# Kernel tuning notes

Hardware: AMD Instinct MI355X
Metric: run time of the kernel (lower is better)

Reference implementation:

```python
import jax, jax.numpy as jnp
import numpy as np

B, T, D, H, N, S, FF = 8, 1024, 512, 8, 256, 256, 2048
AUD, TXT = 768, 256  # audio_input_dim, text_feature_dim (hardcoded in module)
EPS = 1e-5


def _ln(x, g, b):
    m = x.mean(-1, keepdims=True)
    v = ((x - m) ** 2).mean(-1, keepdims=True)
    return (x - m) / jnp.sqrt(v + EPS) * g + b


def _lin(x, w, b):
    return x @ w + b


def setup_inputs() -> dict:
    keys = iter(jax.random.split(jax.random.key(0), 64))
    def rn(shape, s=0.02):
        return jax.random.normal(next(keys), shape, jnp.float32) * s
    inp = {
        'x': jax.random.normal(next(keys), (B, T, D), jnp.float32),
        'xf': jax.random.normal(next(keys), (B, AUD), jnp.float32),
        'xw': jax.random.normal(next(keys), (B, N, TXT), jnp.float32),
        'xs': jax.random.normal(next(keys), (B, S, D), jnp.float32),
        # feat_proj (linear variant)
        'fp_w': rn((D, D)), 'fp_b': rn((D,)),
        # self-attention
        'sa_ng': 1.0 + rn((D,)), 'sa_nb': rn((D,)),
        'sa_qw': rn((D, D)), 'sa_qb': rn((D,)),
        'sa_kw': rn((D, D)), 'sa_kb': rn((D,)),
        'sa_vw': rn((D, D)), 'sa_vb': rn((D,)),
        'sa_ow': rn((D, D)), 'sa_ob': rn((D,)),
        # cross-attention
        'ca_ng': 1.0 + rn((D,)), 'ca_nb': rn((D,)),
        'ca_tng': 1.0 + rn((D,)), 'ca_tnb': rn((D,)),
        'ca_sng': 1.0 + rn((D,)), 'ca_snb': rn((D,)),
        'ca_qw': rn((D, D)), 'ca_qb': rn((D,)),
        'ca_kw': rn((D, D)), 'ca_kb': rn((D,)),
        'ca_vw': rn((D, D)), 'ca_vb': rn((D,)),
        'ca_apw': rn((AUD, TXT)), 'ca_apb': rn((TXT,)),
        'ca_atw': rn((TXT, D)), 'ca_atb': rn((D,)),
        'ca_ow': rn((D, D)), 'ca_ob': rn((D,)),
        'an_g': 1.0 + rn((D,)), 'an_b': rn((D,)),
        # FFN
        'ffn_w1': rn((D, FF)), 'ffn_b1': rn((FF,)),
        'ffn_w2': rn((FF, D)), 'ffn_b2': rn((D,)),
        'ffn_ng': 1.0 + rn((D,)), 'ffn_nb': rn((D,)),
        'ffn_ow': rn((D, D)), 'ffn_ob': rn((D,)),
    }
    return inp


def reference(x, xf, xw, xs, fp_w, fp_b, sa_ng, sa_nb, sa_qw, sa_qb, sa_kw, sa_kb,
              sa_vw, sa_vb, sa_ow, sa_ob, ca_ng, ca_nb, ca_tng, ca_tnb, ca_sng, ca_snb,
              ca_qw, ca_qb, ca_kw, ca_kb, ca_vw, ca_vb, ca_apw, ca_apb, ca_atw, ca_atb,
              ca_ow, ca_ob, an_g, an_b, ffn_w1, ffn_b1, ffn_w2, ffn_b2, ffn_ng, ffn_nb,
              ffn_ow, ffn_ob):
    Bx, Tx, Dx = x.shape
    dh = Dx // H
    # feat_proj + detached residual (x_ori = x.detach().clone())
    xp = _lin(x, fp_w, fp_b) + jax.lax.stop_gradient(x)

    # ---- self-attention block ----
    xn = _ln(xp, sa_ng, sa_nb)
    q = _lin(xn, sa_qw, sa_qb).reshape(Bx, Tx, H, dh)
    k = _lin(xn, sa_kw, sa_kb).reshape(Bx, Tx, H, dh)
    v = _lin(xn, sa_vw, sa_vb).reshape(Bx, Tx, H, dh)
    scores = jnp.einsum('bthd,bshd->bths', q, k) / jnp.sqrt(jnp.float32(dh))
    ao = jnp.einsum('bths,bshd->bthd', jax.nn.softmax(scores, -1), v).reshape(Bx, Tx, Dx)
    sa_out = xp + _lin(jax.nn.silu(ao), sa_ow, sa_ob)
    y1 = _ln(sa_out + xp, an_g, an_b)

    # ---- cross-attention block (linear attention over text/audio + semantic) ----
    Nw = xw.shape[1]
    xf_p = _lin(xf, ca_apw, ca_apb)                              # [B, 256]
    xf_e = jnp.broadcast_to(xf_p[:, None, :], (Bx, Nw, TXT))
    xw_xf = _lin(jnp.concatenate([xw, xf_e], axis=1), ca_atw, ca_atb)  # [B, 2N, D]
    tn = _ln(xw_xf, ca_tng, ca_tnb)
    sn = _ln(xs, ca_sng, ca_snb)
    cq = jax.nn.softmax(_lin(_ln(y1, ca_ng, ca_nb), ca_qw, ca_qb).reshape(Bx, Tx, H, dh), -1)
    ck = jax.nn.softmax(_lin(tn, ca_kw, ca_kb).reshape(Bx, 2 * Nw, H, dh), 1)
    sk = jax.nn.softmax(_lin(sn, ca_kw, ca_kb).reshape(Bx, -1, H, dh), 1)
    cv = _lin(tn, ca_vw, ca_vb).reshape(Bx, 2 * Nw, H, dh)
    sv = _lin(sn, ca_vw, ca_vb).reshape(Bx, -1, H, dh)
    att = jnp.einsum('bnhd,bnhl->bhdl', ck, cv)                  # [B,H,dh,dh]
    satt = jnp.einsum('bshd,bshl->bhsl', sk, sv)                 # [B,H,S,dh]
    cy = jnp.einsum('bthd,bhdl->bthl', cq, att).reshape(Bx, Tx, Dx)
    sy = jnp.einsum('bthd,bhsl->bthl', cq, satt).reshape(Bx, Tx, Dx)
    ca_out = y1 + _lin(jax.nn.silu(cy + sy), ca_ow, ca_ob)
    y2 = _ln(ca_out + y1, an_g, an_b)

    # ---- FFN block ----
    h = jax.nn.gelu(_lin(y2, ffn_w1, ffn_b1), approximate=False)
    h = _ln(_lin(h, ffn_w2, ffn_b2), ffn_ng, ffn_nb)
    ffn_out = y2 + _lin(jax.nn.silu(h), ffn_ow, ffn_ob)
    y3 = _ln(ffn_out + y2, an_g, an_b)
    return y3
```

## Files before the change

kernel.cpp:

```cpp
#include <hip/hip_runtime.h>
#include <math.h>

typedef unsigned short u16;
typedef short s16x8 __attribute__((ext_vector_type(8)));
typedef float f32x4 __attribute__((ext_vector_type(4)));
typedef unsigned short u16x8 __attribute__((ext_vector_type(8)));
typedef unsigned short u16x4 __attribute__((ext_vector_type(4)));

#define DD 512

__device__ __forceinline__ float silu_f(float x) { return x / (1.f + __expf(-x)); }
__device__ __forceinline__ float gelu_f(float x) {
  float y = 1.5957691216f * (x + 0.044715f * x * x * x);
  return x / (1.f + __expf(-y));
}
__device__ __forceinline__ u16 f2bf(float f) {
  unsigned u = __float_as_uint(f);
  return (u16)((u + 0x7fffu + ((u >> 16) & 1u)) >> 16);
}
__device__ __forceinline__ float bf2f(u16 u) { return __uint_as_float(((unsigned)u) << 16); }
__device__ __forceinline__ unsigned cvtpk_bf16(float a, float b) {
  unsigned r;
  asm("v_cvt_pk_bf16_f32 %0, %1, %2" : "=v"(r) : "v"(a), "v"(b));
  return r;
}

__device__ __forceinline__ void gload16(const void* g, void* l) {
  __builtin_amdgcn_global_load_lds(
      (const __attribute__((address_space(1))) void*)(g),
      (__attribute__((address_space(3))) void*)(l), 16, 0, 0);
}

template<int ACT, int OB>
__global__ __launch_bounds__(256) void gemm64(
    const u16* __restrict__ A, const u16* __restrict__ Bt,
    const float* __restrict__ bias, const float* __restrict__ res, float res_scale,
    float* __restrict__ outf, float* __restrict__ outf2,
    u16* __restrict__ outb, u16* __restrict__ outb2,
    int M, int N, int K)
{
  __shared__ u16 As[2][4096];
  __shared__ u16 Bs[2][4096];
  const int t = threadIdx.x, l = t & 63, w = t >> 6;
  const int gx = gridDim.x;
  const int nblk = gx * gridDim.y;
  const int id = blockIdx.y * gx + blockIdx.x;
  const int nid = (id & 7) * (nblk >> 3) + (id >> 3);
  const int bm = (nid / gx) << 6, bn = (nid % gx) << 6;
  const int wr = (w >> 1) << 5, wc = (w & 1) << 5;
  f32x4 acc[2][2];
#pragma unroll
  for (int i = 0; i < 2; ++i)
#pragma unroll
    for (int j = 0; j < 2; ++j) acc[i][j] = (f32x4){0.f, 0.f, 0.f, 0.f};

  auto stage = [&](int k0, int buf) {
#pragma unroll
    for (int i = 0; i < 2; ++i) {
      int c = t + (i << 8);
      int row = c >> 3, cq = c & 7;
      int cs = cq ^ (row & 7);
      gload16(A + (size_t)(bm + row) * K + k0 + cs * 8, (char*)As[buf] + (i << 12) + (w << 10));
      gload16(Bt + (size_t)(bn + row) * K + k0 + cs * 8, (char*)Bs[buf] + (i << 12) + (w << 10));
    }
  };
  stage(0, 0);
  asm volatile("s_waitcnt vmcnt(0)" ::: "memory");
  __builtin_amdgcn_s_barrier();

  const int fr = l & 15, q0 = l >> 4;
  const int nk = K >> 6;
  int cur = 0;
  for (int kt = 0; kt < nk; ++kt) {
    if (kt + 1 < nk) stage((kt + 1) << 6, cur ^ 1);
    s16x8 af[2][2], bg[2][2];
#pragma unroll
    for (int kk = 0; kk < 2; ++kk)
#pragma unroll
      for (int i = 0; i < 2; ++i) {
        int ra = wr + i * 16 + fr;
        af[kk][i] = *(const s16x8*)&As[cur][ra * 64 + (((q0 + kk * 4)) ^ (ra & 7)) * 8];
        int rb = wc + i * 16 + fr;
        bg[kk][i] = *(const s16x8*)&Bs[cur][rb * 64 + (((q0 + kk * 4)) ^ (rb & 7)) * 8];
      }
    asm volatile("s_waitcnt lgkmcnt(0)" ::: "memory");
    __builtin_amdgcn_sched_barrier(0);
#pragma unroll
    for (int kk = 0; kk < 2; ++kk)
#pragma unroll
      for (int mi = 0; mi < 2; ++mi)
#pragma unroll
        for (int ni = 0; ni < 2; ++ni)
          acc[mi][ni] = __builtin_amdgcn_mfma_f32_16x16x32_bf16(af[kk][mi], bg[kk][ni], acc[mi][ni], 0, 0, 0);
    asm volatile("s_waitcnt vmcnt(0)" ::: "memory");
    __builtin_amdgcn_s_barrier();
    cur ^= 1;
  }

  const int cr0 = (l >> 4) << 2, cc = l & 15;

  if (OB == 0 || OB == 4) {
    float* fdst = outf;
    int coff = bn, ld = N;
    if (OB == 4) { ld = 512; coff = bn & 511; if (bn >= 512) fdst = outf2; }
#pragma unroll
    for (int ni = 0; ni < 2; ++ni) {
      int n = bn + wc + ni * 16 + cc;
      int col = coff + wc + ni * 16 + cc;
      float bia = bias[n];
#pragma unroll
      for (int mi = 0; mi < 2; ++mi) {
#pragma unroll
        for (int r = 0; r < 4; ++r) {
          int m = bm + wr + mi * 16 + cr0 + r;
          size_t off = (size_t)m * ld + col;
          float o = acc[mi][ni][r] + bia;
          if (ACT == 1) o = gelu_f(o);
          if (res) o = fmaf(res_scale, res[off], o);
          fdst[off] = o;
        }
      }
    }
  } else if (OB == 1 || OB == 5) {
#pragma unroll
    for (int ni = 0; ni < 2; ++ni) {
      int n = bn + wc + ni * 16 + cc;
      float bia = bias[n];
#pragma unroll
      for (int mi = 0; mi < 2; ++mi) {
#pragma unroll
        for (int r = 0; r < 4; ++r) {
          int m = bm + wr + mi * 16 + cr0 + r;
          size_t off = (size_t)m * N + n;
          float o = acc[mi][ni][r] + bia;
          if (ACT == 1) o = gelu_f(o);
          if (OB == 5) o = fmaf(res_scale, res[off], o);
          outb[off] = f2bf(o);
        }
      }
    }
  } else if (OB == 6) {
    float* smem = (float*)&As[0][0];
    float ev[2][2][4];
    float part[2][4];
#pragma unroll
    for (int mi = 0; mi < 2; ++mi)
#pragma unroll
      for (int r = 0; r < 4; ++r) part[mi][r] = 0.f;
#pragma unroll
    for (int ni = 0; ni < 2; ++ni) {
      float bia = bias[bn + wc + ni * 16 + cc];
#pragma unroll
      for (int mi = 0; mi < 2; ++mi)
#pragma unroll
        for (int r = 0; r < 4; ++r) {
          float e = __expf(acc[mi][ni][r] + bia);
          ev[mi][ni][r] = e;
          part[mi][r] += e;
        }
    }
#pragma unroll
    for (int mi = 0; mi < 2; ++mi)
#pragma unroll
      for (int r = 0; r < 4; ++r) {
        float s = part[mi][r];
        s += __shfl_xor(s, 1); s += __shfl_xor(s, 2);
        s += __shfl_xor(s, 4); s += __shfl_xor(s, 8);
        part[mi][r] = s;
      }
    __syncthreads();
#pragma unroll
    for (int mi = 0; mi < 2; ++mi)
#pragma unroll
      for (int r = 0; r < 4; ++r) {
        int trow = wr + mi * 16 + cr0 + r;
        smem[(w & 1) * 64 + trow] = part[mi][r];
      }
    __syncthreads();
#pragma unroll
    for (int mi = 0; mi < 2; ++mi)
#pragma unroll
      for (int r = 0; r < 4; ++r) {
        int trow = wr + mi * 16 + cr0 + r;
        float inv = 1.f / (smem[trow] + smem[64 + trow]);
#pragma unroll
        for (int ni = 0; ni < 2; ++ni) {
          int n = bn + wc + ni * 16 + cc;
          outb[(size_t)(bm + trow) * 512 + n] = f2bf(ev[mi][ni][r] * inv);
        }
      }
  } else {
    int seg = bn >> 9;
    int colbase = bn & 511;
    if (seg < 2) {
      u16* dst = seg ? outb2 : outb;
#pragma unroll
      for (int ni = 0; ni < 2; ++ni) {
        int col = colbase + wc + ni * 16 + cc;
        float bia = bias[bn + wc + ni * 16 + cc];
#pragma unroll
        for (int mi = 0; mi < 2; ++mi) {
#pragma unroll
          for (int r = 0; r < 4; ++r) {
            int m = bm + wr + mi * 16 + cr0 + r;
            dst[(size_t)m * 512 + col] = f2bf(acc[mi][ni][r] + bia);
          }
        }
      }
    } else {
      u16* tile = &As[0][0];
      __syncthreads();
#pragma unroll
      for (int ni = 0; ni < 2; ++ni) {
        int lc = wc + ni * 16 + cc;
        float bia = bias[bn + wc + ni * 16 + cc];
#pragma unroll
        for (int mi = 0; mi < 2; ++mi) {
          int lm0 = wr + mi * 16 + cr0;
          u16x4 pk;
#pragma unroll
          for (int r = 0; r < 4; ++r) pk[r] = f2bf(acc[mi][ni][r] + bia);
          *(u16x4*)&tile[lc * 64 + (lm0 ^ ((lc & 7) << 3))] = pk;
        }
      }
      __syncthreads();
      int h = colbase >> 6;
      size_t vrow0 = ((size_t)((bm >> 10) * 8 + h)) * 64;
      int d = t >> 3, c8 = (t & 7) << 3;
      *(u16x8*)(((u16*)outf) + (vrow0 + d) * 1024 + (bm & 1023) + c8) =
          *(u16x8*)&tile[d * 64 + (c8 ^ ((d & 7) << 3))];
    }
  }
}

template<int ACT, int OBF>
__global__ __launch_bounds__(512) void gemm8w(
    const u16* __restrict__ A, const u16* __restrict__ Bt,
    const float* __restrict__ bias, float* __restrict__ outf, u16* __restrict__ outb,
    int M, int N, int K)
{
  __shared__ u16 As[2][4096];
  __shared__ u16 Bs[2][8192];
  const int t = threadIdx.x, l = t & 63, w = t >> 6;
  const int gx = gridDim.x;
  const int nblk = gx * gridDim.y;
  const int id = blockIdx.y * gx + blockIdx.x;
  const int nid = (id & 7) * (nblk >> 3) + (id >> 3);
  const int bm = (nid / gx) << 7, bn = (nid % gx) << 8;
  const int wr = (w >> 2) << 6, wc = (w & 3) << 6;
  f32x4 acc[4][4];
#pragma unroll
  for (int i = 0; i < 4; ++i)
#pragma unroll
    for (int j = 0; j < 4; ++j) acc[i][j] = (f32x4){0.f, 0.f, 0.f, 0.f};

  auto stage = [&](int k0, int buf) {
    {
      int row = t >> 2, cq = t & 3;
      int cs = cq ^ ((row >> 1) & 3);
      gload16(A + (size_t)(bm + row) * K + k0 + cs * 8, (char*)As[buf] + (w << 10));
    }
#pragma unroll
    for (int i = 0; i < 2; ++i) {
      int c = t + (i << 9);
      int row = c >> 2, cq = c & 3;
      int cs = cq ^ ((row >> 1) & 3);
      gload16(Bt + (size_t)(bn + row) * K + k0 + cs * 8, (char*)Bs[buf] + ((w + (i << 3)) << 10));
    }
  };
  stage(0, 0);
  asm volatile("s_waitcnt vmcnt(0)" ::: "memory");
  __builtin_amdgcn_s_barrier();

  const int fr = l & 15, q0 = l >> 4;
  const int nk = K >> 5;
  int cur = 0;
  for (int kt = 0; kt < nk; ++kt) {
    if (kt + 1 < nk) stage((kt + 1) << 5, cur ^ 1);
    s16x8 af[4], bg[4];
#pragma unroll
    for (int i = 0; i < 4; ++i) {
      int ra = wr + i * 16 + fr;
      af[i] = *(const s16x8*)&As[cur][ra * 32 + (q0 ^ ((ra >> 1) & 3)) * 8];
      int rb = wc + i * 16 + fr;
      bg[i] = *(const s16x8*)&Bs[cur][rb * 32 + (q0 ^ ((rb >> 1) & 3)) * 8];
    }
    asm volatile("s_waitcnt lgkmcnt(0)" ::: "memory");
    __builtin_amdgcn_sched_barrier(0);
#pragma unroll
    for (int mi = 0; mi < 4; ++mi)
#pragma unroll
      for (int ni = 0; ni < 4; ++ni)
        acc[mi][ni] = __builtin_amdgcn_mfma_f32_16x16x32_bf16(af[mi], bg[ni], acc[mi][ni], 0, 0, 0);
    asm volatile("s_waitcnt vmcnt(0)" ::: "memory");
    __builtin_amdgcn_s_barrier();
    cur ^= 1;
  }

  const int cr0 = (l >> 4) << 2, cc = l & 15;
#pragma unroll
  for (int ni = 0; ni < 4; ++ni) {
    int n = bn + wc + ni * 16 + cc;
    float bia = bias[n];
#pragma unroll
    for (int mi = 0; mi < 4; ++mi) {
#pragma unroll
      for (int r = 0; r < 4; ++r) {
        int m = bm + wr + mi * 16 + cr0 + r;
        size_t off = (size_t)m * N + n;
        float o = acc[mi][ni][r] + bia;
        if (ACT == 1) o = gelu_f(o);
        if (OBF) outb[off] = f2bf(o);
        else outf[off] = o;
      }
    }
  }
}

__global__ __launch_bounds__(256) void xfp_k(
    const float* __restrict__ xf, const u16* __restrict__ apwT,
    const float* __restrict__ bias, float* __restrict__ xfp)
{
  int wid = blockIdx.x * 4 + (threadIdx.x >> 6);
  int lane = threadIdx.x & 63;
  int b = wid >> 8, n = wid & 255;
  const u16* wp = apwT + (size_t)n * 768;
  const float* xp = xf + (size_t)b * 768;
  float s = 0.f;
#pragma unroll
  for (int j = 0; j < 12; ++j) s = fmaf(xp[lane + j * 64], bf2f(wp[lane + j * 64]), s);
#pragma unroll
  for (int m = 1; m < 64; m <<= 1) s += __shfl_xor(s, m);
  if (lane == 0) xfp[wid] = s + bias[n];
}

__global__ __launch_bounds__(256) void biascat_k(
    const float* __restrict__ qb, const float* __restrict__ kb, const float* __restrict__ vb,
    const float* __restrict__ ckb, const float* __restrict__ cvb,
    float* __restrict__ bQKV, float* __restrict__ bKV)
{
  int t = blockIdx.x * 256 + threadIdx.x;
  if (t < 512) bQKV[t] = qb[t];
  else if (t < 1024) bQKV[t] = kb[t - 512];
  else if (t < 1536) bQKV[t] = vb[t - 1024];
  else if (t < 2048) bKV[t - 1536] = ckb[t - 1536];
  else if (t < 2560) bKV[t - 1536] = cvb[t - 2048];
}

__global__ __launch_bounds__(256) void ln_k(
    const float* __restrict__ src, const float* __restrict__ g,
    const float* __restrict__ b, float* __restrict__ out32, u16* __restrict__ out16,
    int rows, int do_silu)
{
  int lane = threadIdx.x & 63, wv = threadIdx.x >> 6;
  int row = (blockIdx.x << 2) + wv;
  if (row >= rows) return;
  const float* p = src + (size_t)row * DD;
  float4 v0 = *(const float4*)(p + lane * 4);
  float4 v1 = *(const float4*)(p + 256 + lane * 4);
  float s = v0.x + v0.y + v0.z + v0.w + v1.x + v1.y + v1.z + v1.w;
  float ss = v0.x*v0.x + v0.y*v0.y + v0.z*v0.z + v0.w*v0.w
           + v1.x*v1.x + v1.y*v1.y + v1.z*v1.z + v1.w*v1.w;
#pragma unroll
  for (int m = 1; m < 64; m <<= 1) { s += __shfl_xor(s, m); ss += __shfl_xor(ss, m); }
  float mean = s * (1.f / 512.f);
  float var = ss * (1.f / 512.f) - mean * mean;
  float rstd = rsqrtf(var + 1e-5f);
  float4 g0 = *(const float4*)(g + lane * 4);
  float4 g1 = *(const float4*)(g + 256 + lane * 4);
  float4 b0 = *(const float4*)(b + lane * 4);
  float4 b1 = *(const float4*)(b + 256 + lane * 4);
  float o[8];
  o[0] = (v0.x - mean) * rstd * g0.x + b0.x;
  o[1] = (v0.y - mean) * rstd * g0.y + b0.y;
  o[2] = (v0.z - mean) * rstd * g0.z + b0.z;
  o[3] = (v0.w - mean) * rstd * g0.w + b0.w;
  o[4] = (v1.x - mean) * rstd * g1.x + b1.x;
  o[5] = (v1.y - mean) * rstd * g1.y + b1.y;
  o[6] = (v1.z - mean) * rstd * g1.z + b1.z;
  o[7] = (v1.w - mean) * rstd * g1.w + b1.w;
  if (do_silu) {
#pragma unroll
    for (int j = 0; j < 8; ++j) o[j] = silu_f(o[j]);
  }
  if (out32) {
    *(float4*)(out32 + (size_t)row * DD + lane * 4) = make_float4(o[0], o[1], o[2], o[3]);
    *(float4*)(out32 + (size_t)row * DD + 256 + lane * 4) = make_float4(o[4], o[5], o[6], o[7]);
  }
  if (out16) {
    u16x4 h0, h1;
#pragma unroll
    for (int j = 0; j < 4; ++j) { h0[j] = f2bf(o[j]); h1[j] = f2bf(o[4 + j]); }
    *(u16x4*)(out16 + (size_t)row * DD + lane * 4) = h0;
    *(u16x4*)(out16 + (size_t)row * DD + 256 + lane * 4) = h1;
  }
}

__global__ __launch_bounds__(256) void lnb_k(
    const u16* __restrict__ src, const float* __restrict__ g,
    const float* __restrict__ b, float* __restrict__ out32, u16* __restrict__ out16,
    int rows, int do_silu)
{
  int lane = threadIdx.x & 63, wv = threadIdx.x >> 6;
  int row = (blockIdx.x << 2) + wv;
  if (row >= rows) return;
  const u16* p = src + (size_t)row * DD;
  u16x4 a0 = *(const u16x4*)(p + lane * 4);
  u16x4 a1 = *(const u16x4*)(p + 256 + lane * 4);
  float v[8];
#pragma unroll
  for (int j = 0; j < 4; ++j) { v[j] = bf2f(a0[j]); v[4 + j] = bf2f(a1[j]); }
  float s = 0.f, ss = 0.f;
#pragma unroll
  for (int j = 0; j < 8; ++j) { s += v[j]; ss = fmaf(v[j], v[j], ss); }
#pragma unroll
  for (int m = 1; m < 64; m <<= 1) { s += __shfl_xor(s, m); ss += __shfl_xor(ss, m); }
  float mean = s * (1.f / 512.f);
  float var = ss * (1.f / 512.f) - mean * mean;
  float rstd = rsqrtf(var + 1e-5f);
  float4 g0 = *(const float4*)(g + lane * 4);
  float4 g1 = *(const float4*)(g + 256 + lane * 4);
  float4 b0 = *(const float4*)(b + lane * 4);
  float4 b1 = *(const float4*)(b + 256 + lane * 4);
  float o[8];
  o[0] = (v[0] - mean) * rstd * g0.x + b0.x;
  o[1] = (v[1] - mean) * rstd * g0.y + b0.y;
  o[2] = (v[2] - mean) * rstd * g0.z + b0.z;
  o[3] = (v[3] - mean) * rstd * g0.w + b0.w;
  o[4] = (v[4] - mean) * rstd * g1.x + b1.x;
  o[5] = (v[5] - mean) * rstd * g1.y + b1.y;
  o[6] = (v[6] - mean) * rstd * g1.z + b1.z;
  o[7] = (v[7] - mean) * rstd * g1.w + b1.w;
  if (do_silu) {
#pragma unroll
    for (int j = 0; j < 8; ++j) o[j] = silu_f(o[j]);
  }
  if (out32) {
    *(float4*)(out32 + (size_t)row * DD + lane * 4) = make_float4(o[0], o[1], o[2], o[3]);
    *(float4*)(out32 + (size_t)row * DD + 256 + lane * 4) = make_float4(o[4], o[5], o[6], o[7]);
  }
  if (out16) {
    u16x4 h0, h1;
#pragma unroll
    for (int j = 0; j < 4; ++j) { h0[j] = f2bf(o[j]); h1[j] = f2bf(o[4 + j]); }
    *(u16x4*)(out16 + (size_t)row * DD + lane * 4) = h0;
    *(u16x4*)(out16 + (size_t)row * DD + 256 + lane * 4) = h1;
  }
}

__global__ __launch_bounds__(256) void ln2_k(
    const u16* __restrict__ src, const float* __restrict__ g1, const float* __restrict__ b1,
    const float* __restrict__ g2, const float* __restrict__ b2,
    float* __restrict__ out1, u16* __restrict__ out2, int rows)
{
  int lane = threadIdx.x & 63, wv = threadIdx.x >> 6;
  int row = (blockIdx.x << 2) + wv;
  if (row >= rows) return;
  const u16* p = src + (size_t)row * DD;
  u16x4 a0 = *(const u16x4*)(p + lane * 4);
  u16x4 a1 = *(const u16x4*)(p + 256 + lane * 4);
  float v[8];
#pragma unroll
  for (int j = 0; j < 4; ++j) { v[j] = bf2f(a0[j]); v[4 + j] = bf2f(a1[j]); }
  float s = 0.f, ss = 0.f;
#pragma unroll
  for (int j = 0; j < 8; ++j) { s += v[j]; ss = fmaf(v[j], v[j], ss); }
#pragma unroll
  for (int m = 1; m < 64; m <<= 1) { s += __shfl_xor(s, m); ss += __shfl_xor(ss, m); }
  float mean = s * (1.f / 512.f);
  float rstd = rsqrtf(ss * (1.f / 512.f) - mean * mean + 1e-5f);
  float4 G0 = *(const float4*)(g1 + lane * 4);
  float4 G1 = *(const float4*)(g1 + 256 + lane * 4);
  float4 B0 = *(const float4*)(b1 + lane * 4);
  float4 B1 = *(const float4*)(b1 + 256 + lane * 4);
  float y[8];
  y[0] = (v[0] - mean) * rstd * G0.x + B0.x;
  y[1] = (v[1] - mean) * rstd * G0.y + B0.y;
  y[2] = (v[2] - mean) * rstd * G0.z + B0.z;
  y[3] = (v[3] - mean) * rstd * G0.w + B0.w;
  y[4] = (v[4] - mean) * rstd * G1.x + B1.x;
  y[5] = (v[5] - mean) * rstd * G1.y + B1.y;
  y[6] = (v[6] - mean) * rstd * G1.z + B1.z;
  y[7] = (v[7] - mean) * rstd * G1.w + B1.w;
  *(float4*)(out1 + (size_t)row * DD + lane * 4) = make_float4(y[0], y[1], y[2], y[3]);
  *(float4*)(out1 + (size_t)row * DD + 256 + lane * 4) = make_float4(y[4], y[5], y[6], y[7]);
  float s2 = 0.f, ss2 = 0.f;
#pragma unroll
  for (int j = 0; j < 8; ++j) { s2 += y[j]; ss2 = fmaf(y[j], y[j], ss2); }
#pragma unroll
  for (int m = 1; m < 64; m <<= 1) { s2 += __shfl_xor(s2, m); ss2 += __shfl_xor(ss2, m); }
  float m2 = s2 * (1.f / 512.f);
  float r2 = rsqrtf(ss2 * (1.f / 512.f) - m2 * m2 + 1e-5f);
  float4 H0 = *(const float4*)(g2 + lane * 4);
  float4 H1 = *(const float4*)(g2 + 256 + lane * 4);
  float4 C0 = *(const float4*)(b2 + lane * 4);
  float4 C1 = *(const float4*)(b2 + 256 + lane * 4);
  u16x4 h0, h1;
  h0[0] = f2bf((y[0] - m2) * r2 * H0.x + C0.x);
  h0[1] = f2bf((y[1] - m2) * r2 * H0.y + C0.y);
  h0[2] = f2bf((y[2] - m2) * r2 * H0.z + C0.z);
  h0[3] = f2bf((y[3] - m2) * r2 * H0.w + C0.w);
  h1[0] = f2bf((y[4] - m2) * r2 * H1.x + C1.x);
  h1[1] = f2bf((y[5] - m2) * r2 * H1.y + C1.y);
  h1[2] = f2bf((y[6] - m2) * r2 * H1.z + C1.z);
  h1[3] = f2bf((y[7] - m2) * r2 * H1.w + C1.w);
  *(u16x4*)(out2 + (size_t)row * DD + lane * 4) = h0;
  *(u16x4*)(out2 + (size_t)row * DD + 256 + lane * 4) = h1;
}

__global__ __launch_bounds__(256) void attn3_k(
    const u16* __restrict__ q, const u16* __restrict__ k,
    const u16* __restrict__ vt, u16* __restrict__ out)
{
  __shared__ __align__(16) char KVb[2][2][8192];
  __shared__ __align__(16) char QP[16384];
  __shared__ float Lr[4][32];

  const int t = threadIdx.x, l = t & 63, w = t >> 6;
  const int id = blockIdx.x;
  const int blk = (id & 7) * 64 + (id >> 3);
  const int qt = blk & 7, h = (blk >> 3) & 7, b = blk >> 6;
  const size_t qbase = ((size_t)(b * 1024 + qt * 128)) * 512 + h * 64;
  const size_t kbase = ((size_t)(b * 1024)) * 512 + h * 64;
  const size_t vbase = ((size_t)((b * 8 + h) * 64)) * 1024;

#pragma unroll
  for (int i = 0; i < 4; ++i) {
    int chunk = i * 256 + w * 64 + l;
    int row = chunk >> 3, c = chunk & 7;
    int cs = c ^ (row & 7);
    gload16(q + qbase + (size_t)row * 512 + cs * 8, QP + (i * 256 + w * 64) * 16);
  }
  auto stageKV = [&](int st, int buf) {
#pragma unroll
    for (int i = 0; i < 2; ++i) {
      int chunk = i * 256 + w * 64 + l;
      int row = chunk >> 3, c = chunk & 7;
      int cs = c ^ (row & 7);
      gload16(k + kbase + (size_t)(st * 64 + row) * 512 + cs * 8,
              KVb[buf][0] + (i * 256 + w * 64) * 16);
      gload16(vt + vbase + (size_t)row * 1024 + st * 64 + cs * 8,
              KVb[buf][1] + (i * 256 + w * 64) * 16);
    }
  };
  stageKV(0, 0);
  __syncthreads();

  s16x8 qf[2][2];
#pragma unroll
  for (int ti = 0; ti < 2; ++ti)
#pragma unroll
    for (int kk = 0; kk < 2; ++kk) {
      int row = w * 32 + ti * 16 + (l & 15);
      int ch = ((l >> 4) + kk * 4) ^ (row & 7);
      qf[ti][kk] = *(const s16x8*)(QP + row * 128 + ch * 16);
    }

  f32x4 oacc[2][4];
#pragma unroll
  for (int qi = 0; qi < 2; ++qi)
#pragma unroll
    for (int dj = 0; dj < 4; ++dj) oacc[qi][dj] = (f32x4){0.f, 0.f, 0.f, 0.f};
  float lsum[2] = {0.f, 0.f};

  int cur = 0;
  for (int st = 0; st < 16; ++st) {
    if (st + 1 < 16) stageKV(st + 1, cur ^ 1);
    f32x4 sacc[4][2];
#pragma unroll
    for (int si = 0; si < 4; ++si)
#pragma unroll
      for (int ti = 0; ti < 2; ++ti) sacc[si][ti] = (f32x4){0.f, 0.f, 0.f, 0.f};
#pragma unroll
    for (int si = 0; si < 4; ++si) {
#pragma unroll
      for (int kk = 0; kk < 2; ++kk) {
        int s = si * 16 + (l & 15);
        int ch = ((l >> 4) + kk * 4) ^ (s & 7);
        s16x8 kf = *(const s16x8*)(KVb[cur][0] + s * 128 + ch * 16);
#pragma unroll
        for (int ti = 0; ti < 2; ++ti)
          sacc[si][ti] = __builtin_amdgcn_mfma_f32_16x16x32_bf16(kf, qf[ti][kk], sacc[si][ti], 0, 0, 0);
      }
    }
#pragma unroll
    for (int si = 0; si < 4; ++si)
#pragma unroll
      for (int ti = 0; ti < 2; ++ti) {
        float e0 = __expf(sacc[si][ti][0] * 0.125f);
        float e1 = __expf(sacc[si][ti][1] * 0.125f);
        float e2 = __expf(sacc[si][ti][2] * 0.125f);
        float e3 = __expf(sacc[si][ti][3] * 0.125f);
        lsum[ti] += (e0 + e1) + (e2 + e3);
        uint2 pk2;
        pk2.x = cvtpk_bf16(e0, e1);
        pk2.y = cvtpk_bf16(e2, e3);
        int tl = ti * 16 + (l & 15);
        int sb = (si * 16 + (l >> 4) * 4) * 2;
        *(uint2*)(QP + w * 4096 + tl * 128 + (sb ^ ((tl & 7) << 4))) = pk2;
      }
#pragma unroll
    for (int kk = 0; kk < 2; ++kk) {
      s16x8 pf[2];
#pragma unroll
      for (int qi = 0; qi < 2; ++qi) {
        int tl = qi * 16 + (l & 15);
        int ch = ((l >> 4) + kk * 4) ^ (tl & 7);
        pf[qi] = *(const s16x8*)(QP + w * 4096 + tl * 128 + ch * 16);
      }
#pragma unroll
      for (int dj = 0; dj < 4; ++dj) {
        int d = dj * 16 + (l & 15);
        int ch = ((l >> 4) + kk * 4) ^ (d & 7);
        s16x8 vf = *(const s16x8*)(KVb[cur][1] + d * 128 + ch * 16);
#pragma unroll
        for (int qi = 0; qi < 2; ++qi)
          oacc[qi][dj] = __builtin_amdgcn_mfma_f32_16x16x32_bf16(pf[qi], vf, oacc[qi][dj], 0, 0, 0);
      }
    }
    cur ^= 1;
    __syncthreads();
  }

#pragma unroll
  for (int ti = 0; ti < 2; ++ti) {
    lsum[ti] += __shfl_xor(lsum[ti], 16);
    lsum[ti] += __shfl_xor(lsum[ti], 32);
    Lr[w][ti * 16 + (l & 15)] = lsum[ti];
  }
  __syncthreads();
  u16* otile = (u16*)QP;
#pragma unroll
  for (int qi = 0; qi < 2; ++qi) {
    float linv[4];
#pragma unroll
    for (int r = 0; r < 4; ++r) linv[r] = 1.f / Lr[w][qi * 16 + (l >> 4) * 4 + r];
#pragma unroll
    for (int dj = 0; dj < 4; ++dj) {
#pragma unroll
      for (int r = 0; r < 4; ++r) {
        int trl = w * 32 + qi * 16 + (l >> 4) * 4 + r;
        otile[trl * 64 + dj * 16 + (l & 15)] = f2bf(silu_f(oacc[qi][dj][r] * linv[r]));
      }
    }
  }
  __syncthreads();
#pragma unroll
  for (int p = 0; p < 4; ++p) {
    int flat = p * 256 + t;
    int row = flat >> 3, c8 = (flat & 7) << 3;
    *(u16x8*)(out + ((size_t)(b * 1024 + qt * 128 + row)) * 512 + h * 64 + c8) =
        *(u16x8*)&otile[row * 64 + c8];
  }
}

__device__ __forceinline__ void smseq_body(float* p, int b, int cg, int NL, int nj, int ci, float* red, int t)
{
  int col = cg * 16 + ci;
  float vals[32];
  float s = 0.f;
  int nit = NL / 16;
  for (int j = 0; j < nit; ++j) {
    float x = __expf(p[((size_t)(b * NL) + nj + j * 16) * 512 + col]);
    vals[j] = x; s += x;
  }
  red[t] = s;
  __syncthreads();
  float tot = 0.f;
#pragma unroll
  for (int j = 0; j < 16; ++j) tot += red[ci + j * 16];
  float inv = 1.f / tot;
  for (int j = 0; j < nit; ++j)
    p[((size_t)(b * NL) + nj + j * 16) * 512 + col] = vals[j] * inv;
}

__global__ __launch_bounds__(256) void smseq2_k(float* __restrict__ ck, float* __restrict__ sk)
{
  __shared__ float red[256];
  int t = threadIdx.x;
  int ci = t & 15, nj = t >> 4;
  if (blockIdx.x < 256) {
    int b = blockIdx.x >> 5, cg = blockIdx.x & 31;
    smseq_body(ck, b, cg, 512, nj, ci, red, t);
  } else {
    int blk = blockIdx.x - 256;
    int b = blk >> 5, cg = blk & 31;
    smseq_body(sk, b, cg, 256, nj, ci, red, t);
  }
}

__global__ __launch_bounds__(256) void build_xc_k(
    const float* __restrict__ xw, const float* __restrict__ xfp, u16* __restrict__ xc)
{
  int idx = blockIdx.x * 256 + threadIdx.x;
  int c = idx & 255, n = (idx >> 8) & 511, b = idx >> 17;
  float val = (n < 256) ? xw[((b << 8) + n) * 256 + c] : xfp[(b << 8) + c];
  xc[idx] = f2bf(val);
}

__global__ __launch_bounds__(256) void attmat1_k(
    const float* __restrict__ ckp, const float* __restrict__ cvp, float* __restrict__ attp)
{
  __shared__ float a_s[64][68];
  __shared__ float b_s[64][68];
  int bh = blockIdx.x >> 3, sl = blockIdx.x & 7;
  int h = bh & 7, b = bh >> 3;
  int n0 = sl << 6;
  int tid = threadIdx.x;
  int d = tid & 63, lg = tid >> 6;
  float acc[16];
#pragma unroll
  for (int j = 0; j < 16; ++j) acc[j] = 0.f;
#pragma unroll
  for (int i = 0; i < 4; ++i) {
    int f = tid + (i << 8);
    int row = f >> 4, c4 = (f & 15) << 2;
    size_t src = ((size_t)(b * 512 + n0 + row)) * DD + h * 64 + c4;
    *(float4*)&a_s[row][c4] = *(const float4*)(ckp + src);
    *(float4*)&b_s[row][c4] = *(const float4*)(cvp + src);
  }
  __syncthreads();
  for (int nn = 0; nn < 64; ++nn) {
    float av = a_s[nn][d];
#pragma unroll
    for (int j4 = 0; j4 < 4; ++j4) {
      float4 b4 = *(float4*)&b_s[nn][lg * 16 + j4 * 4];
      acc[j4*4+0] = fmaf(av, b4.x, acc[j4*4+0]);
      acc[j4*4+1] = fmaf(av, b4.y, acc[j4*4+1]);
      acc[j4*4+2] = fmaf(av, b4.z, acc[j4*4+2]);
      acc[j4*4+3] = fmaf(av, b4.w, acc[j4*4+3]);
    }
  }
  float* op = attp + ((size_t)(bh * 8 + sl)) * 4096 + d * 64 + lg * 16;
#pragma unroll
  for (int j4 = 0; j4 < 4; ++j4)
    *(float4*)(op + j4 * 4) = make_float4(acc[j4*4+0], acc[j4*4+1], acc[j4*4+2], acc[j4*4+3]);
}

__global__ __launch_bounds__(256) void attred_k(
    const float* __restrict__ attp, float* __restrict__ att)
{
  int idx = (blockIdx.x * 256 + threadIdx.x) * 4;
  int bh = idx >> 12, e = idx & 4095;
  float4 s = make_float4(0.f, 0.f, 0.f, 0.f);
#pragma unroll
  for (int sl = 0; sl < 8; ++sl) {
    float4 v = *(const float4*)&attp[((size_t)(bh * 8 + sl)) * 4096 + e];
    s.x += v.x; s.y += v.y; s.z += v.z; s.w += v.w;
  }
  *(float4*)&att[idx] = s;
}

__global__ __launch_bounds__(256) void sy3_k(
    const float* __restrict__ skp, const float* __restrict__ svp, float* __restrict__ sy)
{
  __shared__ float rsum[256];
  __shared__ float part[4][64];
  int b = blockIdx.x >> 3, h = blockIdx.x & 7;
  int t = threadIdx.x;
  int g16 = t >> 4, l16 = t & 15;
  for (int it = 0; it < 16; ++it) {
    int s = g16 * 16 + it;
    const float* base = skp + ((size_t)(b * 256 + s)) * 512 + h * 64;
    float4 v = *(const float4*)(base + l16 * 4);
    float sm = (v.x + v.y) + (v.z + v.w);
    sm += __shfl_xor(sm, 1); sm += __shfl_xor(sm, 2);
    sm += __shfl_xor(sm, 4); sm += __shfl_xor(sm, 8);
    if (l16 == 0) rsum[s] = sm;
  }
  __syncthreads();
  int li = t & 63, sg = t >> 6;
  float acc = 0.f;
  for (int j = 0; j < 64; ++j) {
    int s = sg * 64 + j;
    size_t ix = (size_t)(b * 256 + s);
    acc = fmaf(rsum[s], svp[ix * 512 + h * 64 + li], acc);
  }
  part[sg][li] = acc;
  __syncthreads();
  if (t < 64) sy[(b * 8 + h) * 64 + t] = (part[0][t] + part[1][t]) + (part[2][t] + part[3][t]);
}

__global__ __launch_bounds__(256) void cy_k(
    const u16* __restrict__ cq, const float* __restrict__ att,
    const float* __restrict__ sy, u16* __restrict__ out)
{
  __shared__ float atts[64][68];
  __shared__ float qs[64][68];
  __shared__ float sys[64];
  int blk = blockIdx.x;
  int tt = blk & 15, h = (blk >> 4) & 7, b = blk >> 7;
  int t0 = tt << 6;
  int tid = threadIdx.x;
#pragma unroll
  for (int i = 0; i < 4; ++i) {
    int f = tid + (i << 8);
    int row = f >> 4, c4 = (f & 15) << 2;
    *(float4*)&atts[row][c4] = *(const float4*)(att + (size_t)(b * 8 + h) * 4096 + row * 64 + c4);
    u16x4 qv4 = *(const u16x4*)(cq + ((size_t)(b * 1024 + t0 + row)) * DD + h * 64 + c4);
    qs[row][c4 + 0] = bf2f(qv4[0]);
    qs[row][c4 + 1] = bf2f(qv4[1]);
    qs[row][c4 + 2] = bf2f(qv4[2]);
    qs[row][c4 + 3] = bf2f(qv4[3]);
  }
  if (tid < 64) sys[tid] = sy[(b * 8 + h) * 64 + tid];
  __syncthreads();
  int r = tid >> 2, lg = tid & 3;
  float acc[16];
#pragma unroll
  for (int j = 0; j < 16; ++j) acc[j] = 0.f;
  for (int d = 0; d < 64; ++d) {
    float qv = qs[r][d];
#pragma unroll
    for (int j4 = 0; j4 < 4; ++j4) {
      float4 a4 = *(float4*)&atts[d][lg * 16 + j4 * 4];
      acc[j4*4+0] = fmaf(qv, a4.x, acc[j4*4+0]);
      acc[j4*4+1] = fmaf(qv, a4.y, acc[j4*4+1]);
      acc[j4*4+2] = fmaf(qv, a4.z, acc[j4*4+2]);
      acc[j4*4+3] = fmaf(qv, a4.w, acc[j4*4+3]);
    }
  }
  u16* op = out + ((size_t)(b * 1024 + t0 + r)) * DD + h * 64 + lg * 16;
#pragma unroll
  for (int j4 = 0; j4 < 4; ++j4) {
    u16x4 o4;
    o4[0] = f2bf(silu_f(acc[j4*4+0] + sys[lg * 16 + j4*4+0]));
    o4[1] = f2bf(silu_f(acc[j4*4+1] + sys[lg * 16 + j4*4+1]));
    o4[2] = f2bf(silu_f(acc[j4*4+2] + sys[lg * 16 + j4*4+2]));
    o4[3] = f2bf(silu_f(acc[j4*4+3] + sys[lg * 16 + j4*4+3]));
    *(u16x4*)(op + j4 * 4) = o4;
  }
}

__global__ __launch_bounds__(256) void cvtf2b_k(const float* __restrict__ in, u16* __restrict__ out, int n)
{
  int i = (blockIdx.x * 256 + threadIdx.x) * 4;
  if (i >= n) return;
  float4 v = *(const float4*)(in + i);
  u16x4 o;
  o[0] = f2bf(v.x); o[1] = f2bf(v.y); o[2] = f2bf(v.z); o[3] = f2bf(v.w);
  *(u16x4*)(out + i) = o;
}

struct W10 { const float* w[10]; u16* o[10]; };
__global__ __launch_bounds__(256) void wtrans10_k(W10 p)
{
  __shared__ float tile[32][33];
  int wi = blockIdx.x >> 8;
  int tb = blockIdx.x & 255;
  int tk = tb >> 4, tn = tb & 15;
  const float* W = p.w[wi];
  u16* Wt = p.o[wi];
  int lx = threadIdx.x & 31, ly = threadIdx.x >> 5;
#pragma unroll
  for (int i = 0; i < 4; ++i)
    tile[ly + 8 * i][lx] = W[(size_t)(tk * 32 + ly + 8 * i) * 512 + tn * 32 + lx];
  __syncthreads();
#pragma unroll
  for (int i = 0; i < 4; ++i)
    Wt[(size_t)(tn * 32 + ly + 8 * i) * 512 + tk * 32 + lx] = f2bf(tile[lx][ly + 8 * i]);
}

struct WT4 { const float* w[4]; u16* o[4]; int kd[4]; int nd[4]; int base[4]; };
__global__ __launch_bounds__(256) void wtrans4_k(WT4 p)
{
  __shared__ float tile[32][33];
  int blk = blockIdx.x;
  int e = 3;
  if (blk < p.base[1]) e = 0;
  else if (blk < p.base[2]) e = 1;
  else if (blk < p.base[3]) e = 2;
  int idx = blk - p.base[e];
  const float* W = p.w[e];
  u16* Wt = p.o[e];
  int Kd = p.kd[e], Nd = p.nd[e];
  int ntn = Nd >> 5;
  int tk = idx / ntn, tn = idx % ntn;
  int lx = threadIdx.x & 31, ly = threadIdx.x >> 5;
#pragma unroll
  for (int i = 0; i < 4; ++i)
    tile[ly + 8 * i][lx] = W[(size_t)(tk * 32 + ly + 8 * i) * Nd + tn * 32 + lx];
  __syncthreads();
#pragma unroll
  for (int i = 0; i < 4; ++i)
    Wt[(size_t)(tn * 32 + ly + 8 * i) * Kd + tk * 32 + lx] = f2bf(tile[lx][ly + 8 * i]);
}

extern "C" void kernel_launch(void* const* d_in, const int* in_sizes, int n_in,
                              void* d_out, int out_size, void* d_ws, size_t ws_size,
                              hipStream_t stream)
{
  const float* x      = (const float*)d_in[0];
  const float* xf     = (const float*)d_in[1];
  const float* xw     = (const float*)d_in[2];
  const float* xs     = (const float*)d_in[3];
  const float* fp_w   = (const float*)d_in[4];
  const float* fp_b   = (const float*)d_in[5];
  const float* sa_ng  = (const float*)d_in[6];
  const float* sa_nb  = (const float*)d_in[7];
  const float* sa_qw  = (const float*)d_in[8];
  const float* sa_qb  = (const float*)d_in[9];
  const float* sa_kw  = (const float*)d_in[10];
  const float* sa_kb  = (const float*)d_in[11];
  const float* sa_vw  = (const float*)d_in[12];
  const float* sa_vb  = (const float*)d_in[13];
  const float* sa_ow  = (const float*)d_in[14];
  const float* sa_ob  = (const float*)d_in[15];
  const float* ca_ng  = (const float*)d_in[16];
  const float* ca_nb  = (const float*)d_in[17];
  const float* ca_tng = (const float*)d_in[18];
  const float* ca_tnb = (const float*)d_in[19];
  const float* ca_sng = (const float*)d_in[20];
  const float* ca_snb = (const float*)d_in[21];
  const float* ca_qw  = (const float*)d_in[22];
  const float* ca_qb  = (const float*)d_in[23];
  const float* ca_kw  = (const float*)d_in[24];
  const float* ca_kb  = (const float*)d_in[25];
  const float* ca_vw  = (const float*)d_in[26];
  const float* ca_vb  = (const float*)d_in[27];
  const float* ca_apw = (const float*)d_in[28];
  const float* ca_apb = (const float*)d_in[29];
  const float* ca_atw = (const float*)d_in[30];
  const float* ca_atb = (const float*)d_in[31];
  const float* ca_ow  = (const float*)d_in[32];
  const float* ca_ob  = (const float*)d_in[33];
  const float* an_g   = (const float*)d_in[34];
  const float* an_b   = (const float*)d_in[35];
  const float* ffn_w1 = (const float*)d_in[36];
  const float* ffn_b1 = (const float*)d_in[37];
  const float* ffn_w2 = (const float*)d_in[38];
  const float* ffn_b2 = (const float*)d_in[39];
  const float* ffn_ng = (const float*)d_in[40];
  const float* ffn_nb = (const float*)d_in[41];
  const float* ffn_ow = (const float*)d_in[42];
  const float* ffn_ob = (const float*)d_in[43];

  float* ws = (float*)d_ws;
  float* slotZ = ws;
  float* slotP = ws + 4194304;
  u16* Zb = (u16*)slotZ;
  u16* S1 = (u16*)(ws + 8388608);
  u16* S2 = (u16*)(ws + 10485760);
  u16* S3 = (u16*)(ws + 12582912);
  u16* S4 = (u16*)(ws + 14680064);
  u16* Vt = (u16*)(ws + 16777216);
  u16* S6 = (u16*)(ws + 18874368);
  float* ck  = ws + 20971520;
  float* sk  = ws + 23068672;
  float* cv  = ws + 24117248;
  float* sv  = ws + 26214400;
  float* tnr = ws + 27262976;
  u16* tn = (u16*)(ws + 29360128);
  u16* sn = (u16*)(ws + 30408704);
  u16* h1 = (u16*)(ws + 20971520);
  u16* xc = (u16*)(ws + 30932992);
  float* att = ws + 31457280;
  float* xfp = ws + 31719424;
  float* sy  = ws + 31723520;
  u16* wb = (u16*)(ws + 31727616);
  u16* fp_wt   = wb;
  u16* sa_qwt  = wb + 262144;
  u16* sa_kwt  = wb + 524288;
  u16* sa_vwt  = wb + 786432;
  u16* sa_owt  = wb + 1048576;
  u16* ca_qwt  = wb + 1310720;
  u16* ca_kwt  = wb + 1572864;
  u16* ca_vwt  = wb + 1835008;
  u16* ca_owt  = wb + 2097152;
  u16* ffn_owt = wb + 2359296;
  u16* ca_atwt = wb + 2621440;
  u16* ffn_w1t = wb + 2752512;
  u16* ffn_w2t = wb + 3801088;
  u16* apwT    = wb + 4849664;
  float* bQKV  = (float*)(wb + 5046272);
  float* bKV   = bQKV + 1536;
  float* attp  = ws + 34260992;

  dim3 blk(256);
  auto g64 = [](int M, int N) { return dim3((unsigned)(N >> 6), (unsigned)(M >> 6)); };

  cvtf2b_k<<<dim3(4096), blk, 0, stream>>>(x, S1, 4194304);
  W10 wp;
  wp.w[0] = fp_w;  wp.o[0] = fp_wt;
  wp.w[1] = sa_qw; wp.o[1] = sa_qwt;
  wp.w[2] = sa_kw; wp.o[2] = sa_kwt;
  wp.w[3] = sa_vw; wp.o[3] = sa_vwt;
  wp.w[4] = sa_ow; wp.o[4] = sa_owt;
  wp.w[5] = ca_qw; wp.o[5] = ca_qwt;
  wp.w[6] = ca_kw; wp.o[6] = ca_kwt;
  wp.w[7] = ca_vw; wp.o[7] = ca_vwt;
  wp.w[8] = ca_ow; wp.o[8] = ca_owt;
  wp.w[9] = ffn_ow; wp.o[9] = ffn_owt;
  wtrans10_k<<<dim3(2560), blk, 0, stream>>>(wp);
  WT4 wq;
  wq.w[0] = ca_atw; wq.o[0] = ca_atwt; wq.kd[0] = 256;  wq.nd[0] = 512;  wq.base[0] = 0;
  wq.w[1] = ffn_w1; wq.o[1] = ffn_w1t; wq.kd[1] = 512;  wq.nd[1] = 2048; wq.base[1] = 128;
  wq.w[2] = ffn_w2; wq.o[2] = ffn_w2t; wq.kd[2] = 2048; wq.nd[2] = 512;  wq.base[2] = 1152;
  wq.w[3] = ca_apw; wq.o[3] = apwT;    wq.kd[3] = 768;  wq.nd[3] = 256;  wq.base[3] = 2176;
  wtrans4_k<<<dim3(2368), blk, 0, stream>>>(wq);
  biascat_k<<<dim3(10), blk, 0, stream>>>(sa_qb, sa_kb, sa_vb, ca_kb, ca_vb, bQKV, bKV);

  xfp_k<<<dim3(512), blk, 0, stream>>>(xf, apwT, ca_apb, xfp);
  build_xc_k<<<dim3(4096), blk, 0, stream>>>(xw, xfp, xc);
  gemm64<0,0><<<g64(4096, 512), blk, 0, stream>>>(xc, ca_atwt, ca_atb, nullptr, 0.f, tnr, nullptr, nullptr, nullptr, 4096, 512, 256);
  ln_k<<<dim3(1024), blk, 0, stream>>>(tnr, ca_tng, ca_tnb, nullptr, tn, 4096, 0);
  ln_k<<<dim3(512), blk, 0, stream>>>(xs, ca_sng, ca_snb, nullptr, sn, 2048, 0);

  gemm64<0,0><<<g64(8192, 512), blk, 0, stream>>>(S1, fp_wt, fp_b, x, 1.f, slotP, nullptr, nullptr, nullptr, 8192, 512, 512);
  ln_k<<<dim3(2048), blk, 0, stream>>>(slotP, sa_ng, sa_nb, nullptr, S2, 8192, 0);
  gemm64<0,3><<<g64(8192, 1536), blk, 0, stream>>>(S2, sa_qwt, bQKV, nullptr, 0.f, (float*)Vt, nullptr, S3, S4, 8192, 1536, 512);
  attn3_k<<<dim3(512), blk, 0, stream>>>(S3, S4, Vt, S6);
  gemm64<0,5><<<g64(8192, 512), blk, 0, stream>>>(S6, sa_owt, sa_ob, slotP, 2.f, nullptr, nullptr, Zb, nullptr, 8192, 512, 512);
  ln2_k<<<dim3(2048), blk, 0, stream>>>(Zb, an_g, an_b, ca_ng, ca_nb, slotP, S1, 8192);

  gemm64<0,6><<<g64(8192, 512), blk, 0, stream>>>(S1, ca_qwt, ca_qb, nullptr, 0.f, nullptr, nullptr, Zb, nullptr, 8192, 512, 512);
  gemm64<0,4><<<g64(6144, 1024), blk, 0, stream>>>(tn, ca_kwt, bKV, nullptr, 0.f, ck, cv, nullptr, nullptr, 6144, 1024, 512);
  smseq2_k<<<dim3(512), blk, 0, stream>>>(ck, sk);
  attmat1_k<<<dim3(512), blk, 0, stream>>>(ck, cv, attp);
  attred_k<<<dim3(256), blk, 0, stream>>>(attp, att);
  sy3_k<<<dim3(64), blk, 0, stream>>>(sk, sv, sy);
  cy_k<<<dim3(1024), blk, 0, stream>>>(Zb, att, sy, S2);
  gemm64<0,5><<<g64(8192, 512), blk, 0, stream>>>(S2, ca_owt, ca_ob, slotP, 2.f, nullptr, nullptr, Zb, nullptr, 8192, 512, 512);
  lnb_k<<<dim3(2048), blk, 0, stream>>>(Zb, an_g, an_b, slotP, S3, 8192, 0);

  gemm8w<1,1><<<dim3(8, 64), dim3(512), 0, stream>>>(S3, ffn_w1t, ffn_b1, nullptr, h1, 8192, 2048, 512);
  gemm64<0,1><<<g64(8192, 512), blk, 0, stream>>>(h1, ffn_w2t, ffn_b2, nullptr, 0.f, nullptr, nullptr, Zb, nullptr, 8192, 512, 2048);
  lnb_k<<<dim3(2048), blk, 0, stream>>>(Zb, ffn_ng, ffn_nb, nullptr, S1, 8192, 1);
  gemm64<0,5><<<g64(8192, 512), blk, 0, stream>>>(S1, ffn_owt, ffn_ob, slotP, 2.f, nullptr, nullptr, Zb, nullptr, 8192, 512, 512);
  lnb_k<<<dim3(2048), blk, 0, stream>>>(Zb, an_g, an_b, (float*)d_out, nullptr, 8192, 0);
}
```

Measured before the change: 330.6 us.

## Load attention K/V fragments directly from global memory instead of LDS staging

The self-attention kernel no longer double-buffers K and V^T tiles through shared memory. Each wave now reads its MFMA K and V fragments straight from global memory into registers, and the per-iteration block barrier is removed. This cuts LDS use from about 48KB to about 16KB per block, which may raise occupancy and removes synchronization overhead. In exchange, K/V loads are duplicated across the four waves and rely on L1/L2 hits, and load latency is exposed directly in front of the MFMAs with no explicit prefetch.

Measured after the change: 371.8 us. 12.5% more time.

```diff
diff --git a/kernel.cpp b/kernel.cpp
--- a/kernel.cpp
+++ b/kernel.cpp
@@ -508,11 +508,10 @@
   *(u16x4*)(out2 + (size_t)row * DD + 256 + lane * 4) = h1;
 }
 
-__global__ __launch_bounds__(256) void attn3_k(
+__global__ __launch_bounds__(256) void attn4_k(
     const u16* __restrict__ q, const u16* __restrict__ k,
     const u16* __restrict__ vt, u16* __restrict__ out)
 {
-  __shared__ __align__(16) char KVb[2][2][8192];
   __shared__ __align__(16) char QP[16384];
   __shared__ float Lr[4][32];
 
@@ -531,20 +530,8 @@
     int cs = c ^ (row & 7);
     gload16(q + qbase + (size_t)row * 512 + cs * 8, QP + (i * 256 + w * 64) * 16);
   }
-  auto stageKV = [&](int st, int buf) {
-#pragma unroll
-    for (int i = 0; i < 2; ++i) {
-      int chunk = i * 256 + w * 64 + l;
-      int row = chunk >> 3, c = chunk & 7;
-      int cs = c ^ (row & 7);
-      gload16(k + kbase + (size_t)(st * 64 + row) * 512 + cs * 8,
-              KVb[buf][0] + (i * 256 + w * 64) * 16);
-      gload16(vt + vbase + (size_t)row * 1024 + st * 64 + cs * 8,
-              KVb[buf][1] + (i * 256 + w * 64) * 16);
-    }
-  };
-  stageKV(0, 0);
-  __syncthreads();
+  asm volatile("s_waitcnt vmcnt(0)" ::: "memory");
+  __builtin_amdgcn_s_barrier();
 
   s16x8 qf[2][2];
 #pragma unroll
@@ -555,6 +542,8 @@
       int ch = ((l >> 4) + kk * 4) ^ (row & 7);
       qf[ti][kk] = *(const s16x8*)(QP + row * 128 + ch * 16);
     }
+  asm volatile("s_waitcnt lgkmcnt(0)" ::: "memory");
+  __builtin_amdgcn_s_barrier();
 
   f32x4 oacc[2][4];
 #pragma unroll
@@ -563,9 +552,9 @@
     for (int dj = 0; dj < 4; ++dj) oacc[qi][dj] = (f32x4){0.f, 0.f, 0.f, 0.f};
   float lsum[2] = {0.f, 0.f};
 
-  int cur = 0;
+  const int fr16 = l & 15, q16 = l >> 4;
+
   for (int st = 0; st < 16; ++st) {
-    if (st + 1 < 16) stageKV(st + 1, cur ^ 1);
     f32x4 sacc[4][2];
 #pragma unroll
     for (int si = 0; si < 4; ++si)
@@ -573,14 +562,13 @@
       for (int ti = 0; ti < 2; ++ti) sacc[si][ti] = (f32x4){0.f, 0.f, 0.f, 0.f};
 #pragma unroll
     for (int si = 0; si < 4; ++si) {
-#pragma unroll
-      for (int kk = 0; kk < 2; ++kk) {
-        int s = si * 16 + (l & 15);
-        int ch = ((l >> 4) + kk * 4) ^ (s & 7);
-        s16x8 kf = *(const s16x8*)(KVb[cur][0] + s * 128 + ch * 16);
-#pragma unroll
-        for (int ti = 0; ti < 2; ++ti)
-          sacc[si][ti] = __builtin_amdgcn_mfma_f32_16x16x32_bf16(kf, qf[ti][kk], sacc[si][ti], 0, 0, 0);
+      const u16* kp = k + kbase + (size_t)(st * 64 + si * 16 + fr16) * 512 + q16 * 8;
+      s16x8 kf0 = *(const s16x8*)(kp);
+      s16x8 kf1 = *(const s16x8*)(kp + 32);
+#pragma unroll
+      for (int ti = 0; ti < 2; ++ti) {
+        sacc[si][ti] = __builtin_amdgcn_mfma_f32_16x16x32_bf16(kf0, qf[ti][0], sacc[si][ti], 0, 0, 0);
+        sacc[si][ti] = __builtin_amdgcn_mfma_f32_16x16x32_bf16(kf1, qf[ti][1], sacc[si][ti], 0, 0, 0);
       }
     }
 #pragma unroll
@@ -610,16 +598,13 @@
       }
 #pragma unroll
       for (int dj = 0; dj < 4; ++dj) {
-        int d = dj * 16 + (l & 15);
-        int ch = ((l >> 4) + kk * 4) ^ (d & 7);
-        s16x8 vf = *(const s16x8*)(KVb[cur][1] + d * 128 + ch * 16);
+        const u16* vp = vt + vbase + (size_t)(dj * 16 + fr16) * 1024 + st * 64 + (q16 + kk * 4) * 8;
+        s16x8 vf = *(const s16x8*)(vp);
 #pragma unroll
         for (int qi = 0; qi < 2; ++qi)
           oacc[qi][dj] = __builtin_amdgcn_mfma_f32_16x16x32_bf16(pf[qi], vf, oacc[qi][dj], 0, 0, 0);
       }
     }
-    cur ^= 1;
-    __syncthreads();
   }
 
 #pragma unroll
@@ -628,7 +613,7 @@
     lsum[ti] += __shfl_xor(lsum[ti], 32);
     Lr[w][ti * 16 + (l & 15)] = lsum[ti];
   }
-  __syncthreads();
+  asm volatile("s_waitcnt lgkmcnt(0)" ::: "memory");
   u16* otile = (u16*)QP;
 #pragma unroll
   for (int qi = 0; qi < 2; ++qi) {
@@ -1009,7 +994,7 @@
   gemm64<0,0><<<g64(8192, 512), blk, 0, stream>>>(S1, fp_wt, fp_b, x, 1.f, slotP, nullptr, nullptr, nullptr, 8192, 512, 512);
   ln_k<<<dim3(2048), blk, 0, stream>>>(slotP, sa_ng, sa_nb, nullptr, S2, 8192, 0);
   gemm64<0,3><<<g64(8192, 1536), blk, 0, stream>>>(S2, sa_qwt, bQKV, nullptr, 0.f, (float*)Vt, nullptr, S3, S4, 8192, 1536, 512);
-  attn3_k<<<dim3(512), blk, 0, stream>>>(S3, S4, Vt, S6);
+  attn4_k<<<dim3(512), blk, 0, stream>>>(S3, S4, Vt, S6);
   gemm64<0,5><<<g64(8192, 512), blk, 0, stream>>>(S6, sa_owt, sa_ob, slotP, 2.f, nullptr, nullptr, Zb, nullptr, 8192, 512, 512);
   ln2_k<<<dim3(2048), blk, 0, stream>>>(Zb, an_g, an_b, ca_ng, ca_nb, slotP, S1, 8192);
 
```
